# Performance work log

Hardware: AMD Instinct MI355X
Metric: run time of the kernel (lower is better)

Reference implementation:

```python
import jax, jax.numpy as jnp
import numpy as np

NUM_MIXTURES = 10
DIM_INPUT = 512
DIM_FEATURES = 512
SEQ_LEN = 512
BATCH = 16
NUM_CHAR = 1024
DIM_CONTEXT = 256


def setup_inputs() -> dict:
    key = jax.random.key(0)
    ks = jax.random.split(key, 6)
    inputs = jax.random.normal(ks[0], (SEQ_LEN, BATCH, DIM_INPUT), dtype=jnp.float32)
    context_vectors = jax.random.normal(ks[1], (NUM_CHAR, BATCH, DIM_CONTEXT), dtype=jnp.float32)
    init_means = jnp.zeros((BATCH, NUM_MIXTURES), dtype=jnp.float32)
    # StackedLinearLayers params: 2 layers, leaky_relu between, out dim = 3*K
    s1 = 1.0 / np.sqrt(DIM_INPUT)
    s2 = 1.0 / np.sqrt(DIM_FEATURES)
    W1 = jax.random.uniform(ks[2], (DIM_INPUT, DIM_FEATURES), jnp.float32, -s1, s1)
    b1 = jax.random.uniform(ks[3], (DIM_FEATURES,), jnp.float32, -s1, s1)
    W2 = jax.random.uniform(ks[4], (DIM_FEATURES, 3 * NUM_MIXTURES), jnp.float32, -s2, s2)
    b2 = jax.random.uniform(ks[5], (3 * NUM_MIXTURES,), jnp.float32, -s2, s2)
    return dict(inputs=inputs, context_vectors=context_vectors, init_means=init_means,
                W1=W1, b1=b1, W2=W2, b2=b2, extra_chars=0)


def reference(inputs, context_vectors, init_means, W1, b1, W2, b2, extra_chars):
    K = NUM_MIXTURES
    seq_len, batch, _ = inputs.shape
    num_char = context_vectors.shape[0]
    total_char = num_char + extra_chars

    # StackedLinearLayers: leaky_relu MLP, last layer linear -> (S, B, 3K)
    h = jax.nn.leaky_relu(inputs @ W1 + b1, negative_slope=0.01)
    outs = h @ W2 + b2
    outs = jax.nn.softplus(outs)  # pos_fun = softplus

    delta_means, vars_, weights = jnp.split(outs, 3, axis=2)  # each (S, B, K)
    delta_means = delta_means / 25.0
    vars_ = jnp.clip(vars_, 0.01, 100.0)
    means = jnp.cumsum(delta_means, axis=0) + init_means[None, :, :]  # (S, B, K)

    cidxs = jnp.arange(total_char, dtype=jnp.float32)  # (T,)
    # dists: (S, B, K, T)
    dists = -((means[..., None] - cidxs) ** 2) * vars_[..., None]
    # attn_weights = exp(logsumexp over mixtures)
    attn_weights = jnp.exp(
        jax.scipy.special.logsumexp(jnp.log(weights)[..., None] + dists, axis=2)
    )  # (S, B, T)

    # attended contexts: (S, B, D)
    attn_contexts = jnp.einsum('sbc,cbd->sbd', attn_weights[:, :, :num_char], context_vectors)
    return attn_contexts, attn_weights, means, vars_, weights
```

## Files before the change

### kernel.cpp

```cpp
#include <hip/hip_runtime.h>
#include <math.h>

#define S_LEN 512
#define BATCH 16
#define DIN   512
#define DF    512
#define NMIX  10
#define NCHAR 1024
#define DCTX  256
#define M_ROWS (S_LEN*BATCH)

#define OFF_CTXOUT 0
#define OFF_ATTN   (S_LEN*BATCH*DCTX)
#define OFF_MEANS  (OFF_ATTN + S_LEN*BATCH*NCHAR)
#define OFF_VARS   (OFF_MEANS + S_LEN*BATCH*NMIX)
#define OFF_WTS    (OFF_VARS  + S_LEN*BATCH*NMIX)

#define WS_XH    0
#define WS_W1T   (8u<<20)
#define WS_W2T   (9u<<20)
#define WS_HH    (10u<<20)
#define WS_ATTNH (26u<<20)
#define WS_BOUND (44u<<20)

#define NX4     1048576
#define CVT_BLOCKS (NX4/256)
#define W1T_BLOCKS 64
#define W2T_BLOCKS 64

typedef float    f32x16 __attribute__((ext_vector_type(16)));
typedef float    f32x4v __attribute__((ext_vector_type(4)));
typedef _Float16 f16x8  __attribute__((ext_vector_type(8)));

__device__ __forceinline__ unsigned short f2h(float x) {
    union { _Float16 h; unsigned short u; } cv;
    cv.h = (_Float16)x;
    return cv.u;
}
__device__ __forceinline__ ushort4 cvt4(float4 v) {
    ushort4 o; o.x = f2h(v.x); o.y = f2h(v.y); o.z = f2h(v.z); o.w = f2h(v.w);
    return o;
}
__device__ __forceinline__ void nt_store4(float* p, float a, float b, float c, float d) {
    f32x4v v; v.x = a; v.y = b; v.z = c; v.w = d;
    __builtin_nontemporal_store(v, (f32x4v*)p);
}

__global__ __launch_bounds__(256) void convert_kernel(
    const float* __restrict__ X, const float* __restrict__ W1,
    const float* __restrict__ W2,
    unsigned short* __restrict__ Xh, unsigned short* __restrict__ W1T,
    float* __restrict__ W2T, unsigned int* __restrict__ bound)
{
    const int bid = blockIdx.x;
    const int tid = threadIdx.x;
    if (bid < CVT_BLOCKS) {
        const int i4 = bid*256 + tid;
        ((ushort4*)Xh)[i4] = cvt4(((const float4*)X)[i4]);
    } else if (bid < CVT_BLOCKS + W1T_BLOCKS) {
        __shared__ unsigned short tile[64*68];
        const int b2 = bid - CVT_BLOCKS;
        const int k0 = (b2 >> 3) * 64, n0 = (b2 & 7) * 64;
        #pragma unroll
        for (int q = 0; q < 4; q++) {
            const int r = q*16 + (tid >> 4);
            const int c = (tid & 15) * 4;
            float4 v = *(const float4*)(W1 + (size_t)(k0+r)*DF + n0 + c);
            *(ushort4*)(tile + r*68 + c) = cvt4(v);
        }
        __syncthreads();
        #pragma unroll
        for (int q = 0; q < 4; q++) {
            const int n  = q*16 + (tid >> 4);
            const int kq = (tid & 15) * 4;
            ushort4 o;
            o.x = tile[(kq+0)*68 + n];
            o.y = tile[(kq+1)*68 + n];
            o.z = tile[(kq+2)*68 + n];
            o.w = tile[(kq+3)*68 + n];
            *(ushort4*)(W1T + (size_t)(n0+n)*DIN + k0 + kq) = o;
        }
    } else if (bid < CVT_BLOCKS + W1T_BLOCKS + W2T_BLOCKS) {
        const int idx = (bid - CVT_BLOCKS - W1T_BLOCKS)*256 + tid;
        if (idx < 512*32) {
            const int j = idx >> 9, k = idx & 511;
            W2T[idx] = (j < 30) ? W2[k*30 + j] : 0.f;
        }
    } else {
        if (tid < BATCH*8) bound[tid] = 0u;
    }
}

__global__ __launch_bounds__(256) void gemm1_kernel(
    const unsigned short* __restrict__ Xh, const unsigned short* __restrict__ W1T,
    const float* __restrict__ b1, unsigned short* __restrict__ Hh)
{
    __shared__ __align__(16) unsigned short As[64*72];
    __shared__ __align__(16) unsigned short Bs[64*72];
    const int row0 = (blockIdx.x >> 3) * 64;
    const int n0   = (blockIdx.x & 7)  * 64;
    const int tid  = threadIdx.x;
    const int lane = tid & 63, w = tid >> 6;
    const int wr = (w >> 1) * 32, wc = (w & 1) * 32;
    const int m  = lane & 31,  g  = lane >> 5;
    const int sa = tid >> 2,   ka = (tid & 3) * 16;

    f32x16 acc = {};
    const unsigned short* aptr = Xh  + (size_t)(row0+sa)*DIN + ka;
    const unsigned short* bptr = W1T + (size_t)(n0 +sa)*DIN + ka;

    for (int kt = 0; kt < DIN; kt += 64) {
        uint4 av0 = *(const uint4*)(aptr + kt);
        uint4 av1 = *(const uint4*)(aptr + kt + 8);
        uint4 bv0 = *(const uint4*)(bptr + kt);
        uint4 bv1 = *(const uint4*)(bptr + kt + 8);
        __syncthreads();
        *(uint4*)(As + sa*72 + ka)     = av0;
        *(uint4*)(As + sa*72 + ka + 8) = av1;
        *(uint4*)(Bs + sa*72 + ka)     = bv0;
        *(uint4*)(Bs + sa*72 + ka + 8) = bv1;
        __syncthreads();
        #pragma unroll
        for (int ks = 0; ks < 64; ks += 16) {
            f16x8 af = *(const f16x8*)(As + (wr+m)*72 + ks + g*8);
            f16x8 bf = *(const f16x8*)(Bs + (wc+m)*72 + ks + g*8);
            acc = __builtin_amdgcn_mfma_f32_32x32x16_f16(af, bf, acc, 0, 0, 0);
        }
    }
    const int ncol = n0 + wc + m;
    const float bb = b1[ncol];
    #pragma unroll
    for (int r = 0; r < 16; r++) {
        const int rowloc = (r & 3) + 8*(r >> 2) + 4*g;
        const int row = row0 + wr + rowloc;
        float v = acc[r] + bb;
        v = v > 0.f ? v : 0.01f * v;
        Hh[(size_t)row*DF + ncol] = f2h(v);
    }
}

__global__ __launch_bounds__(256) void gemm2_kernel(
    const unsigned short* __restrict__ Hh, const float* __restrict__ W2T,
    const float* __restrict__ b2,
    float* __restrict__ dmeans, float* __restrict__ dvars, float* __restrict__ dwts)
{
    __shared__ __align__(16) unsigned short Hs[32*520];
    const int tid = threadIdx.x;
    const int r0  = blockIdx.x * 32;
    {
        const uint4* src = (const uint4*)(Hh + (size_t)r0*DF);
        #pragma unroll
        for (int i = 0; i < 8; i++) {
            int u   = tid + i*256;
            int row = u >> 6;
            int col = (u & 63) * 8;
            *(uint4*)(Hs + row*520 + col) = src[u];
        }
    }
    __syncthreads();

    const int r  = tid & 31;
    const int j0 = tid >> 5;
    const unsigned short* hrow = Hs + r*520;
    float acc[4] = {0.f, 0.f, 0.f, 0.f};

    for (int k0 = 0; k0 < DF; k0 += 8) {
        union { uint4 u; _Float16 h[8]; } hv;
        hv.u = *(const uint4*)(hrow + k0);
        float wv[4][8];
        #pragma unroll
        for (int q = 0; q < 4; q++) {
            *(float4*)(wv[q])     = *(const float4*)(W2T + (size_t)(j0 + q*8)*DF + k0);
            *(float4*)(wv[q] + 4) = *(const float4*)(W2T + (size_t)(j0 + q*8)*DF + k0 + 4);
        }
        #pragma unroll
        for (int i = 0; i < 8; i++) {
            float hf = (float)hv.h[i];
            acc[0] = fmaf(hf, wv[0][i], acc[0]);
            acc[1] = fmaf(hf, wv[1][i], acc[1]);
            acc[2] = fmaf(hf, wv[2][i], acc[2]);
            acc[3] = fmaf(hf, wv[3][i], acc[3]);
        }
    }
    const int row = r0 + r;
    #pragma unroll
    for (int q = 0; q < 4; q++) {
        const int j = j0 + q*8;
        if (j >= 30) continue;
        float dot = acc[q] + b2[j];
        float sp  = fmaxf(dot, 0.f) + log1pf(__expf(-fabsf(dot)));
        if (j < 10)       dmeans[row*NMIX + j]      = sp / 25.0f;
        else if (j < 20)  dvars [row*NMIX + (j-10)] = fminf(fmaxf(sp, 0.01f), 100.f);
        else              dwts  [row*NMIX + (j-20)] = sp;
    }
}

__global__ __launch_bounds__(512) void scan_kernel(
    const float* __restrict__ init_means, float* __restrict__ means,
    const float* __restrict__ vars_g, unsigned int* __restrict__ bound)
{
    const int p    = blockIdx.x;
    const int s    = threadIdx.x;
    const int lane = s & 63;
    const int wid  = s >> 6;

    float x = means[s*(BATCH*NMIX) + p];
    #pragma unroll
    for (int d = 1; d < 64; d <<= 1) {
        float tv = __shfl_up(x, d, 64);
        if (lane >= d) x += tv;
    }
    __shared__ float wsum[8];
    if (lane == 63) wsum[wid] = x;
    __syncthreads();
    float off = init_means[p];
    for (int i = 0; i < wid; i++) off += wsum[i];
    x += off;
    means[s*(BATCH*NMIX) + p] = x;

    float v = vars_g[s*(BATCH*NMIX) + p];
    float reach = x + 4.8f * rsqrtf(v);
    #pragma unroll
    for (int d = 32; d >= 1; d >>= 1)
        reach = fmaxf(reach, __shfl_xor(reach, d, 64));
    if (lane == 0)
        atomicMax((int*)&bound[(p / NMIX) * 8 + wid], __float_as_int(reach));
}

__global__ __launch_bounds__(256) void attn_kernel(
    const float* __restrict__ means, const float* __restrict__ vars,
    const float* __restrict__ wts,   const unsigned int* __restrict__ bound,
    float* __restrict__ attn, unsigned short* __restrict__ attnh)
{
    const int row = blockIdx.x;
    const int b   = row & (BATCH-1);
    const int tid = threadIdx.x;
    const int bd  = (int)__int_as_float((int)bound[b*8 + (row >> 10)]);
    const int kmax = min(NCHAR, (bd + 64) & ~63);
    const int t0  = tid * 4;

    float o[4] = {0.f, 0.f, 0.f, 0.f};
    if (t0 <= bd) {
        float m[NMIX], v[NMIX], w[NMIX];
        #pragma unroll
        for (int k = 0; k < NMIX; k++) {
            m[k] = means[row*NMIX + k];
            v[k] = vars [row*NMIX + k];
            w[k] = wts  [row*NMIX + k];
        }
        #pragma unroll
        for (int i = 0; i < 4; i++) {
            const float t = (float)(t0 + i);
            float sum = 0.f;
            #pragma unroll
            for (int k = 0; k < NMIX; k++) {
                float d = t - m[k];
                sum += w[k] * __expf(-d*d*v[k]);
            }
            o[i] = sum;
        }
    }
    nt_store4(attn + (size_t)row*NCHAR + t0, o[0], o[1], o[2], o[3]);
    if (t0 < kmax) {
        ushort4 h; h.x = f2h(o[0]); h.y = f2h(o[1]); h.z = f2h(o[2]); h.w = f2h(o[3]);
        *(ushort4*)(attnh + (size_t)row*NCHAR + t0) = h;
    }
}

__global__ __launch_bounds__(256) void ctx_mfma_kernel(
    const unsigned short* __restrict__ attnh, const float* __restrict__ ctx,
    const unsigned int* __restrict__ bound, float* __restrict__ out)
{
    __shared__ __align__(16) unsigned short As[64*72];
    __shared__ __align__(16) unsigned short Bs[64*72];
    const int bid  = blockIdx.x;
    const int b    = bid >> 5;
    const int rem  = bid & 31;
    const int s0   = (rem >> 2) * 64;
    const int d0   = (rem & 3)  * 64;
    const int tid  = threadIdx.x;
    const int lane = tid & 63, w = tid >> 6;
    const int wr = (w >> 1) * 32, wc = (w & 1) * 32;
    const int m  = lane & 31,  g  = lane >> 5;
    const int sl = tid >> 2,   tq = (tid & 3) * 16;
    const int tb = tid & 63,   db = (tid >> 6) * 16;

    const int bd   = (int)__int_as_float((int)bound[b*8 + (rem >> 2)]);
    const int kmax = min(NCHAR, (bd + 64) & ~63);

    f32x16 acc = {};
    const unsigned short* abase = attnh + (size_t)(s0+sl)*(BATCH*NCHAR) + b*NCHAR + tq;
    const float*          bbase = ctx   + (size_t)b*DCTX + d0 + db;

    for (int kt = 0; kt < kmax; kt += 64) {
        uint4 a0  = *(const uint4*)(abase + kt);
        uint4 a1  = *(const uint4*)(abase + kt + 8);
        float4 bf0 = *(const float4*)(bbase + (size_t)(kt+tb)*(BATCH*DCTX));
        float4 bf1 = *(const float4*)(bbase + (size_t)(kt+tb)*(BATCH*DCTX) + 4);
        float4 bf2 = *(const float4*)(bbase + (size_t)(kt+tb)*(BATCH*DCTX) + 8);
        float4 bf3 = *(const float4*)(bbase + (size_t)(kt+tb)*(BATCH*DCTX) + 12);
        __syncthreads();
        *(uint4*)(As + sl*72 + tq)     = a0;
        *(uint4*)(As + sl*72 + tq + 8) = a1;
        {
            ushort4 h0 = cvt4(bf0), h1 = cvt4(bf1), h2 = cvt4(bf2), h3 = cvt4(bf3);
            Bs[(db + 0)*72 + tb] = h0.x;  Bs[(db + 1)*72 + tb] = h0.y;
            Bs[(db + 2)*72 + tb] = h0.z;  Bs[(db + 3)*72 + tb] = h0.w;
            Bs[(db + 4)*72 + tb] = h1.x;  Bs[(db + 5)*72 + tb] = h1.y;
            Bs[(db + 6)*72 + tb] = h1.z;  Bs[(db + 7)*72 + tb] = h1.w;
            Bs[(db + 8)*72 + tb] = h2.x;  Bs[(db + 9)*72 + tb] = h2.y;
            Bs[(db +10)*72 + tb] = h2.z;  Bs[(db +11)*72 + tb] = h2.w;
            Bs[(db +12)*72 + tb] = h3.x;  Bs[(db +13)*72 + tb] = h3.y;
            Bs[(db +14)*72 + tb] = h3.z;  Bs[(db +15)*72 + tb] = h3.w;
        }
        __syncthreads();
        #pragma unroll
        for (int ks = 0; ks < 64; ks += 16) {
            f16x8 af = *(const f16x8*)(As + (wr+m)*72 + ks + g*8);
            f16x8 bf = *(const f16x8*)(Bs + (wc+m)*72 + ks + g*8);
            acc = __builtin_amdgcn_mfma_f32_32x32x16_f16(af, bf, acc, 0, 0, 0);
        }
    }
    #pragma unroll
    for (int r = 0; r < 16; r++) {
        int rowloc = (r & 3) + 8*(r >> 2) + 4*g;
        int s = s0 + wr + rowloc;
        __builtin_nontemporal_store(acc[r],
            out + (size_t)s*(BATCH*DCTX) + b*DCTX + d0 + wc + m);
    }
}

extern "C" void kernel_launch(void* const* d_in, const int* in_sizes, int n_in,
                              void* d_out, int out_size, void* d_ws, size_t ws_size,
                              hipStream_t stream)
{
    const float* X     = (const float*)d_in[0];
    const float* ctx   = (const float*)d_in[1];
    const float* initm = (const float*)d_in[2];
    const float* W1    = (const float*)d_in[3];
    const float* b1    = (const float*)d_in[4];
    const float* W2    = (const float*)d_in[5];
    const float* b2    = (const float*)d_in[6];

    float* out      = (float*)d_out;
    float* out_ctx  = out + OFF_CTXOUT;
    float* out_attn = out + OFF_ATTN;
    float* out_mean = out + OFF_MEANS;
    float* out_var  = out + OFF_VARS;
    float* out_wts  = out + OFF_WTS;

    char* ws = (char*)d_ws;
    unsigned short* Xh    = (unsigned short*)(ws + WS_XH);
    unsigned short* W1T   = (unsigned short*)(ws + WS_W1T);
    float*          W2T   = (float*)         (ws + WS_W2T);
    unsigned short* Hh    = (unsigned short*)(ws + WS_HH);
    unsigned short* attnh = (unsigned short*)(ws + WS_ATTNH);
    unsigned int*   bnd   = (unsigned int*)  (ws + WS_BOUND);

    convert_kernel<<<CVT_BLOCKS + W1T_BLOCKS + W2T_BLOCKS + 1, 256, 0, stream>>>(
        X, W1, W2, Xh, W1T, W2T, bnd);
    gemm1_kernel<<<(M_ROWS/64)*(DF/64), 256, 0, stream>>>(Xh, W1T, b1, Hh);
    gemm2_kernel<<<M_ROWS/32, 256, 0, stream>>>(Hh, W2T, b2, out_mean, out_var, out_wts);
    scan_kernel<<<BATCH*NMIX, 512, 0, stream>>>(initm, out_mean, out_var, bnd);
    attn_kernel<<<M_ROWS, 256, 0, stream>>>(out_mean, out_var, out_wts, bnd,
                                            out_attn, attnh);
    ctx_mfma_kernel<<<16*8*4, 256, 0, stream>>>(attnh, ctx, bnd, out_ctx);
}
```

Before: 144.2 us.

## Fuse scan, attention weights and context GEMM into one kernel

Replaces the scan, attn and ctx_mfma kernels with one fused kernel. Each block handles 32 timesteps of one batch element. It recomputes the prefix carry from a transposed delta-means buffer, computes attention weights per 64-char tile straight into LDS as fp16, and feeds them to MFMA against the context. This removes the fp16 attention round-trip through global memory, the atomic bound buffer and two launches. In exchange there are only 256 blocks, each block re-reads its prefix chain, and each tile now does serial exp work before its MFMA.

```diff
diff --git a/kernel.cpp b/kernel.cpp
--- a/kernel.cpp
+++ b/kernel.cpp
@@ -20,8 +20,7 @@
 #define WS_W1T   (8u<<20)
 #define WS_W2T   (9u<<20)
 #define WS_HH    (10u<<20)
-#define WS_ATTNH (26u<<20)
-#define WS_BOUND (44u<<20)
+#define WS_DM    (26u<<20)
 
 #define NX4     1048576
 #define CVT_BLOCKS (NX4/256)
@@ -50,7 +49,7 @@
     const float* __restrict__ X, const float* __restrict__ W1,
     const float* __restrict__ W2,
     unsigned short* __restrict__ Xh, unsigned short* __restrict__ W1T,
-    float* __restrict__ W2T, unsigned int* __restrict__ bound)
+    float* __restrict__ W2T)
 {
     const int bid = blockIdx.x;
     const int tid = threadIdx.x;
@@ -80,14 +79,12 @@
             o.w = tile[(kq+3)*68 + n];
             *(ushort4*)(W1T + (size_t)(n0+n)*DIN + k0 + kq) = o;
         }
-    } else if (bid < CVT_BLOCKS + W1T_BLOCKS + W2T_BLOCKS) {
+    } else {
         const int idx = (bid - CVT_BLOCKS - W1T_BLOCKS)*256 + tid;
         if (idx < 512*32) {
             const int j = idx >> 9, k = idx & 511;
             W2T[idx] = (j < 30) ? W2[k*30 + j] : 0.f;
         }
-    } else {
-        if (tid < BATCH*8) bound[tid] = 0u;
     }
 }
 
@@ -142,7 +139,7 @@
 __global__ __launch_bounds__(256) void gemm2_kernel(
     const unsigned short* __restrict__ Hh, const float* __restrict__ W2T,
     const float* __restrict__ b2,
-    float* __restrict__ dmeans, float* __restrict__ dvars, float* __restrict__ dwts)
+    float* __restrict__ dm_ws, float* __restrict__ dvars, float* __restrict__ dwts)
 {
     __shared__ __align__(16) unsigned short Hs[32*520];
     const int tid = threadIdx.x;
@@ -189,144 +186,153 @@
         if (j >= 30) continue;
         float dot = acc[q] + b2[j];
         float sp  = fmaxf(dot, 0.f) + log1pf(__expf(-fabsf(dot)));
-        if (j < 10)       dmeans[row*NMIX + j]      = sp / 25.0f;
-        else if (j < 20)  dvars [row*NMIX + (j-10)] = fminf(fmaxf(sp, 0.01f), 100.f);
-        else              dwts  [row*NMIX + (j-20)] = sp;
-    }
-}
-
-__global__ __launch_bounds__(512) void scan_kernel(
-    const float* __restrict__ init_means, float* __restrict__ means,
-    const float* __restrict__ vars_g, unsigned int* __restrict__ bound)
-{
-    const int p    = blockIdx.x;
-    const int s    = threadIdx.x;
-    const int lane = s & 63;
-    const int wid  = s >> 6;
-
-    float x = means[s*(BATCH*NMIX) + p];
-    #pragma unroll
-    for (int d = 1; d < 64; d <<= 1) {
-        float tv = __shfl_up(x, d, 64);
-        if (lane >= d) x += tv;
-    }
-    __shared__ float wsum[8];
-    if (lane == 63) wsum[wid] = x;
+        if (j < 10) {
+            const int bb = row & (BATCH-1), s = row >> 4;
+            dm_ws[((size_t)bb*NMIX + j)*S_LEN + s] = sp * (1.f/25.f);
+        }
+        else if (j < 20)  dvars[row*NMIX + (j-10)] = fminf(fmaxf(sp, 0.01f), 100.f);
+        else              dwts [row*NMIX + (j-20)] = sp;
+    }
+}
+
+__global__ __launch_bounds__(256) void fused_kernel(
+    const float* __restrict__ dm_ws, const float* __restrict__ init_means,
+    const float* __restrict__ vars_g, const float* __restrict__ wts_g,
+    const float* __restrict__ ctx,
+    float* __restrict__ means_out, float* __restrict__ attn_out,
+    float* __restrict__ ctxout)
+{
+    __shared__ float mlds[320];
+    __shared__ float vlds[320];
+    __shared__ float wlds[320];
+    __shared__ float redbuf[4];
+    __shared__ __align__(16) unsigned short As[32*72];
+    __shared__ __align__(16) unsigned short Bs[256*72];
+
+    const int bid = blockIdx.x;
+    const int b   = bid >> 4;
+    const int s0  = (bid & 15) * 32;
+    const int tid = threadIdx.x;
+    const int lane = tid & 63, w = tid >> 6;
+    const int m = lane & 31, g = lane >> 5;
+
+    for (int k = w; k < NMIX; k += 4) {
+        const float* chain = dm_ws + ((size_t)b*NMIX + k)*S_LEN;
+        float part = 0.f;
+        for (int s = lane; s < s0; s += 64) part += chain[s];
+        #pragma unroll
+        for (int d = 32; d >= 1; d >>= 1) part += __shfl_xor(part, d, 64);
+        const float carry = init_means[b*NMIX + k] + part;
+        float v = (lane < 32) ? chain[s0 + lane] : 0.f;
+        #pragma unroll
+        for (int d = 1; d < 32; d <<= 1) {
+            float t = __shfl_up(v, d, 64);
+            if (lane >= d) v += t;
+        }
+        if (lane < 32) mlds[lane*NMIX + k] = carry + v;
+    }
+    for (int idx = tid; idx < 320; idx += 256) {
+        const int s = idx / NMIX, k = idx - s*NMIX;
+        const int row = (s0 + s)*BATCH + b;
+        vlds[idx] = vars_g[row*NMIX + k];
+        wlds[idx] = wts_g [row*NMIX + k];
+    }
     __syncthreads();
-    float off = init_means[p];
-    for (int i = 0; i < wid; i++) off += wsum[i];
-    x += off;
-    means[s*(BATCH*NMIX) + p] = x;
-
-    float v = vars_g[s*(BATCH*NMIX) + p];
-    float reach = x + 4.8f * rsqrtf(v);
-    #pragma unroll
-    for (int d = 32; d >= 1; d >>= 1)
-        reach = fmaxf(reach, __shfl_xor(reach, d, 64));
-    if (lane == 0)
-        atomicMax((int*)&bound[(p / NMIX) * 8 + wid], __float_as_int(reach));
-}
-
-__global__ __launch_bounds__(256) void attn_kernel(
-    const float* __restrict__ means, const float* __restrict__ vars,
-    const float* __restrict__ wts,   const unsigned int* __restrict__ bound,
-    float* __restrict__ attn, unsigned short* __restrict__ attnh)
-{
-    const int row = blockIdx.x;
-    const int b   = row & (BATCH-1);
-    const int tid = threadIdx.x;
-    const int bd  = (int)__int_as_float((int)bound[b*8 + (row >> 10)]);
-    const int kmax = min(NCHAR, (bd + 64) & ~63);
-    const int t0  = tid * 4;
-
-    float o[4] = {0.f, 0.f, 0.f, 0.f};
-    if (t0 <= bd) {
-        float m[NMIX], v[NMIX], w[NMIX];
-        #pragma unroll
-        for (int k = 0; k < NMIX; k++) {
-            m[k] = means[row*NMIX + k];
-            v[k] = vars [row*NMIX + k];
-            w[k] = wts  [row*NMIX + k];
-        }
-        #pragma unroll
-        for (int i = 0; i < 4; i++) {
-            const float t = (float)(t0 + i);
+
+    float reach = 0.f;
+    for (int idx = tid; idx < 320; idx += 256) {
+        const int s = idx / NMIX, k = idx - s*NMIX;
+        means_out[((s0 + s)*BATCH + b)*NMIX + k] = mlds[idx];
+        reach = fmaxf(reach, mlds[idx] + 4.8f * rsqrtf(vlds[idx]));
+    }
+    #pragma unroll
+    for (int d = 32; d >= 1; d >>= 1) reach = fmaxf(reach, __shfl_xor(reach, d, 64));
+    if (lane == 0) redbuf[w] = reach;
+    __syncthreads();
+    const float rmax = fmaxf(fmaxf(redbuf[0], redbuf[1]),
+                             fmaxf(redbuf[2], redbuf[3]));
+    const int kmax = min(NCHAR, (((int)rmax) + 64) & ~63);
+
+    const int r  = tid >> 3;
+    const int c0 = (tid & 7) * 8;
+    float mr[NMIX], vr[NMIX], wr_[NMIX];
+    #pragma unroll
+    for (int k = 0; k < NMIX; k++) {
+        mr[k]  = mlds[r*NMIX + k];
+        vr[k]  = vlds[r*NMIX + k];
+        wr_[k] = wlds[r*NMIX + k];
+    }
+    const size_t arow = (size_t)((s0 + r)*BATCH + b) * NCHAR;
+
+    const int tb = tid & 63, dseg = tid >> 6;
+    const float* cbase = ctx + (size_t)b*DCTX + dseg*64;
+
+    f32x16 acc0 = {}, acc1 = {};
+    for (int kt = 0; kt < kmax; kt += 64) {
+        float o[8];
+        #pragma unroll
+        for (int i = 0; i < 8; i++) {
+            const float t = (float)(kt + c0 + i);
             float sum = 0.f;
             #pragma unroll
             for (int k = 0; k < NMIX; k++) {
-                float d = t - m[k];
-                sum += w[k] * __expf(-d*d*v[k]);
+                float d = t - mr[k];
+                sum += wr_[k] * __expf(-d*d*vr[k]);
             }
             o[i] = sum;
         }
-    }
-    nt_store4(attn + (size_t)row*NCHAR + t0, o[0], o[1], o[2], o[3]);
-    if (t0 < kmax) {
-        ushort4 h; h.x = f2h(o[0]); h.y = f2h(o[1]); h.z = f2h(o[2]); h.w = f2h(o[3]);
-        *(ushort4*)(attnh + (size_t)row*NCHAR + t0) = h;
-    }
-}
-
-__global__ __launch_bounds__(256) void ctx_mfma_kernel(
-    const unsigned short* __restrict__ attnh, const float* __restrict__ ctx,
-    const unsigned int* __restrict__ bound, float* __restrict__ out)
-{
-    __shared__ __align__(16) unsigned short As[64*72];
-    __shared__ __align__(16) unsigned short Bs[64*72];
-    const int bid  = blockIdx.x;
-    const int b    = bid >> 5;
-    const int rem  = bid & 31;
-    const int s0   = (rem >> 2) * 64;
-    const int d0   = (rem & 3)  * 64;
-    const int tid  = threadIdx.x;
-    const int lane = tid & 63, w = tid >> 6;
-    const int wr = (w >> 1) * 32, wc = (w & 1) * 32;
-    const int m  = lane & 31,  g  = lane >> 5;
-    const int sl = tid >> 2,   tq = (tid & 3) * 16;
-    const int tb = tid & 63,   db = (tid >> 6) * 16;
-
-    const int bd   = (int)__int_as_float((int)bound[b*8 + (rem >> 2)]);
-    const int kmax = min(NCHAR, (bd + 64) & ~63);
-
-    f32x16 acc = {};
-    const unsigned short* abase = attnh + (size_t)(s0+sl)*(BATCH*NCHAR) + b*NCHAR + tq;
-    const float*          bbase = ctx   + (size_t)b*DCTX + d0 + db;
-
-    for (int kt = 0; kt < kmax; kt += 64) {
-        uint4 a0  = *(const uint4*)(abase + kt);
-        uint4 a1  = *(const uint4*)(abase + kt + 8);
-        float4 bf0 = *(const float4*)(bbase + (size_t)(kt+tb)*(BATCH*DCTX));
-        float4 bf1 = *(const float4*)(bbase + (size_t)(kt+tb)*(BATCH*DCTX) + 4);
-        float4 bf2 = *(const float4*)(bbase + (size_t)(kt+tb)*(BATCH*DCTX) + 8);
-        float4 bf3 = *(const float4*)(bbase + (size_t)(kt+tb)*(BATCH*DCTX) + 12);
-        __syncthreads();
-        *(uint4*)(As + sl*72 + tq)     = a0;
-        *(uint4*)(As + sl*72 + tq + 8) = a1;
+        __syncthreads();
+        nt_store4(attn_out + arow + kt + c0,     o[0], o[1], o[2], o[3]);
+        nt_store4(attn_out + arow + kt + c0 + 4, o[4], o[5], o[6], o[7]);
         {
-            ushort4 h0 = cvt4(bf0), h1 = cvt4(bf1), h2 = cvt4(bf2), h3 = cvt4(bf3);
-            Bs[(db + 0)*72 + tb] = h0.x;  Bs[(db + 1)*72 + tb] = h0.y;
-            Bs[(db + 2)*72 + tb] = h0.z;  Bs[(db + 3)*72 + tb] = h0.w;
-            Bs[(db + 4)*72 + tb] = h1.x;  Bs[(db + 5)*72 + tb] = h1.y;
-            Bs[(db + 6)*72 + tb] = h1.z;  Bs[(db + 7)*72 + tb] = h1.w;
-            Bs[(db + 8)*72 + tb] = h2.x;  Bs[(db + 9)*72 + tb] = h2.y;
-            Bs[(db +10)*72 + tb] = h2.z;  Bs[(db +11)*72 + tb] = h2.w;
-            Bs[(db +12)*72 + tb] = h3.x;  Bs[(db +13)*72 + tb] = h3.y;
-            Bs[(db +14)*72 + tb] = h3.z;  Bs[(db +15)*72 + tb] = h3.w;
+            ushort4 h0, h1;
+            h0.x = f2h(o[0]); h0.y = f2h(o[1]); h0.z = f2h(o[2]); h0.w = f2h(o[3]);
+            h1.x = f2h(o[4]); h1.y = f2h(o[5]); h1.z = f2h(o[6]); h1.w = f2h(o[7]);
+            *(ushort4*)(As + r*72 + c0)     = h0;
+            *(ushort4*)(As + r*72 + c0 + 4) = h1;
+        }
+        {
+            const float* p = cbase + (size_t)(kt + tb)*(BATCH*DCTX);
+            #pragma unroll
+            for (int e = 0; e < 4; e++) {
+                float4 f0 = *(const float4*)(p + e*16);
+                float4 f1 = *(const float4*)(p + e*16 + 4);
+                float4 f2 = *(const float4*)(p + e*16 + 8);
+                float4 f3 = *(const float4*)(p + e*16 + 12);
+                ushort4 h0 = cvt4(f0), h1 = cvt4(f1), h2 = cvt4(f2), h3 = cvt4(f3);
+                const int db = dseg*64 + e*16;
+                Bs[(db + 0)*72 + tb] = h0.x;  Bs[(db + 1)*72 + tb] = h0.y;
+                Bs[(db + 2)*72 + tb] = h0.z;  Bs[(db + 3)*72 + tb] = h0.w;
+                Bs[(db + 4)*72 + tb] = h1.x;  Bs[(db + 5)*72 + tb] = h1.y;
+                Bs[(db + 6)*72 + tb] = h1.z;  Bs[(db + 7)*72 + tb] = h1.w;
+                Bs[(db + 8)*72 + tb] = h2.x;  Bs[(db + 9)*72 + tb] = h2.y;
+                Bs[(db +10)*72 + tb] = h2.z;  Bs[(db +11)*72 + tb] = h2.w;
+                Bs[(db +12)*72 + tb] = h3.x;  Bs[(db +13)*72 + tb] = h3.y;
+                Bs[(db +14)*72 + tb] = h3.z;  Bs[(db +15)*72 + tb] = h3.w;
+            }
         }
         __syncthreads();
         #pragma unroll
         for (int ks = 0; ks < 64; ks += 16) {
-            f16x8 af = *(const f16x8*)(As + (wr+m)*72 + ks + g*8);
-            f16x8 bf = *(const f16x8*)(Bs + (wc+m)*72 + ks + g*8);
-            acc = __builtin_amdgcn_mfma_f32_32x32x16_f16(af, bf, acc, 0, 0, 0);
-        }
-    }
-    #pragma unroll
-    for (int r = 0; r < 16; r++) {
-        int rowloc = (r & 3) + 8*(r >> 2) + 4*g;
-        int s = s0 + wr + rowloc;
-        __builtin_nontemporal_store(acc[r],
-            out + (size_t)s*(BATCH*DCTX) + b*DCTX + d0 + wc + m);
+            f16x8 af  = *(const f16x8*)(As + m*72 + ks + g*8);
+            f16x8 bf0 = *(const f16x8*)(Bs + (w*64 + m)*72      + ks + g*8);
+            f16x8 bf1 = *(const f16x8*)(Bs + (w*64 + 32 + m)*72 + ks + g*8);
+            acc0 = __builtin_amdgcn_mfma_f32_32x32x16_f16(af, bf0, acc0, 0, 0, 0);
+            acc1 = __builtin_amdgcn_mfma_f32_32x32x16_f16(af, bf1, acc1, 0, 0, 0);
+        }
+    }
+    for (int t = kmax + c0; t < NCHAR; t += 64) {
+        nt_store4(attn_out + arow + t,     0.f, 0.f, 0.f, 0.f);
+        nt_store4(attn_out + arow + t + 4, 0.f, 0.f, 0.f, 0.f);
+    }
+
+    #pragma unroll
+    for (int rr = 0; rr < 16; rr++) {
+        const int rowloc = (rr & 3) + 8*(rr >> 2) + 4*g;
+        const int s = s0 + rowloc;
+        float* op = ctxout + ((size_t)s*BATCH + b)*DCTX + w*64 + m;
+        __builtin_nontemporal_store(acc0[rr], op);
+        __builtin_nontemporal_store(acc1[rr], op + 32);
     }
 }
 
@@ -350,19 +356,16 @@
     float* out_wts  = out + OFF_WTS;
 
     char* ws = (char*)d_ws;
-    unsigned short* Xh    = (unsigned short*)(ws + WS_XH);
-    unsigned short* W1T   = (unsigned short*)(ws + WS_W1T);
-    float*          W2T   = (float*)         (ws + WS_W2T);
-    unsigned short* Hh    = (unsigned short*)(ws + WS_HH);
-    unsigned short* attnh = (unsigned short*)(ws + WS_ATTNH);
-    unsigned int*   bnd   = (unsigned int*)  (ws + WS_BOUND);
-
-    convert_kernel<<<CVT_BLOCKS + W1T_BLOCKS + W2T_BLOCKS + 1, 256, 0, stream>>>(
-        X, W1, W2, Xh, W1T, W2T, bnd);
+    unsigned short* Xh   = (unsigned short*)(ws + WS_XH);
+    unsigned short* W1T  = (unsigned short*)(ws + WS_W1T);
+    float*          W2T  = (float*)         (ws + WS_W2T);
+    unsigned short* Hh   = (unsigned short*)(ws + WS_HH);
+    float*          dmws = (float*)         (ws + WS_DM);
+
+    convert_kernel<<<CVT_BLOCKS + W1T_BLOCKS + W2T_BLOCKS, 256, 0, stream>>>(
+        X, W1, W2, Xh, W1T, W2T);
     gemm1_kernel<<<(M_ROWS/64)*(DF/64), 256, 0, stream>>>(Xh, W1T, b1, Hh);
-    gemm2_kernel<<<M_ROWS/32, 256, 0, stream>>>(Hh, W2T, b2, out_mean, out_var, out_wts);
-    scan_kernel<<<BATCH*NMIX, 512, 0, stream>>>(initm, out_mean, out_var, bnd);
-    attn_kernel<<<M_ROWS, 256, 0, stream>>>(out_mean, out_var, out_wts, bnd,
-                                            out_attn, attnh);
-    ctx_mfma_kernel<<<16*8*4, 256, 0, stream>>>(attnh, ctx, bnd, out_ctx);
-}
+    gemm2_kernel<<<M_ROWS/32, 256, 0, stream>>>(Hh, W2T, b2, dmws, out_var, out_wts);
+    fused_kernel<<<BATCH*16, 256, 0, stream>>>(dmws, initm, out_var, out_wts, ctx,
+                                               out_mean, out_attn, out_ctx);
+}
```

Result: no change. 145.7 us (+1.1%).
